# Kernel tuning notes

Measured on AMD Instinct MI355X. Metric: run time of the kernel, lower is better.

The kernel has to match this reference:

```python
import jax, jax.numpy as jnp
import numpy as np

N, DX, DZ, DY, H = 8192, 64, 128, 16, 512


def setup_inputs() -> dict:
    key = jax.random.key(0)
    ks = jax.random.split(key, 8)
    s1 = 1.0 / np.sqrt(DX)
    s2 = 1.0 / np.sqrt(H)
    return {
        "z_pred": jax.random.normal(ks[0], (N, DZ), dtype=jnp.float32),
        "x_label": jax.random.normal(ks[1], (N, DX), dtype=jnp.float32),
        "y_label": jax.random.normal(ks[2], (N, DY), dtype=jnp.float32),
        "W1": jax.random.normal(ks[3], (DX, H), dtype=jnp.float32) * s1,
        "b1": jnp.zeros((H,), dtype=jnp.float32),
        "W2": jax.random.normal(ks[4], (H, DZ), dtype=jnp.float32) * s2,
        "b2": jnp.zeros((DZ,), dtype=jnp.float32),
        "A": jax.random.normal(ks[5], (DZ, DZ), dtype=jnp.float32) * (1.0 / np.sqrt(DZ)),
        "B": jax.random.normal(ks[6], (DZ, DY), dtype=jnp.float32) * (1.0 / np.sqrt(DY)),
    }


def reference(z_pred, x_label, y_label, W1, b1, W2, b2, A, B):
    # forward_mapper T: x (dx,) -> (dz,), 2-layer tanh MLP
    def T(x):
        return jnp.tanh(x @ W1 + b1) @ W2 + b2

    # diff_eq: per-sample nonlinear dynamics x_dot = tanh(x)
    x_dot = jnp.tanh(x_label)  # (N, dx)

    # per-sample Jacobian dT/dx: (N, dz, dx). Equivalent to the torch code's
    # full N x N batched Jacobian followed by the diagonal slice, but without
    # the O(N^2) waste.
    jac = jax.vmap(jax.jacrev(T))(x_label)  # (N, dz, dx)

    dtdx_mul_f = jnp.einsum("nzd,nd->nz", jac, x_dot)  # (N, dz)
    m_mul_t = z_pred @ A.T                              # (N, dz)
    k_mul_h = y_label @ B.T                             # (N, dz)

    pde = dtdx_mul_f - m_mul_t - k_mul_h                # (N, dz)
    loss_batch = jnp.linalg.norm(pde, axis=1)           # (N,)
    return jnp.mean(loss_batch)
```

## Files before the change

### kernel.cpp

```cpp
#include <hip/hip_runtime.h>
#include <math.h>

#define Nn   8192
#define DXc  64
#define DZc  128
#define DYc  16
#define Hc   512
#define NKC  21

typedef short bf16x8 __attribute__((ext_vector_type(8)));
typedef float f32x4  __attribute__((ext_vector_type(4)));

__device__ __forceinline__ float fast_tanh(float x) {
    float e = __expf(2.0f * x);
    return 1.0f - 2.0f / (e + 1.0f);
}
__device__ __forceinline__ short f2bf(float f) {
    unsigned u = __float_as_uint(f);
    return (short)((u + 0x7FFFu + ((u >> 16) & 1u)) >> 16);
}
__device__ __forceinline__ bf16x8 pack8(float4 a, float4 b) {
    bf16x8 r;
    r[0]=f2bf(a.x); r[1]=f2bf(a.y); r[2]=f2bf(a.z); r[3]=f2bf(a.w);
    r[4]=f2bf(b.x); r[5]=f2bf(b.y); r[6]=f2bf(b.z); r[7]=f2bf(b.w);
    return r;
}

__global__ void prep_kernel(const float* __restrict__ W1,
                            const float* __restrict__ W2,
                            const float* __restrict__ A,
                            const float* __restrict__ Bm,
                            short* __restrict__ Wb,
                            short* __restrict__ Wf) {
    __shared__ float tile[64 * 129];
    const int blk = blockIdx.x, t = threadIdx.x;

    if (blk < 8) {
        const int jb = blk * 64;
#pragma unroll
        for (int p = 0; p < 16; p++) {
            int lin = p * 256 + t;
            int k = lin >> 6, jj = lin & 63;
            tile[jj * 65 + k] = W1[(size_t)k * Hc + jb + jj];
        }
        __syncthreads();
#pragma unroll
        for (int p = 0; p < 2; p++) {
            int cid = p * 256 + t;
            int lane = cid & 63, q = lane >> 4, n16 = lane & 15;
            int kc2 = (cid >> 6) & 1, jt4 = cid >> 7;
            int jl = jt4 * 16 + n16, k0 = kc2 * 32 + q * 8;
            bf16x8 v;
#pragma unroll
            for (int i = 0; i < 8; i++) v[i] = f2bf(tile[jl * 65 + k0 + i]);
            int block = ((blk * 4 + jt4) * 2 + kc2);
            *(bf16x8*)(Wb + (size_t)(block * 64 + lane) * 8) = v;
        }
    } else if (blk < 16) {
        const int kb = (blk - 8) * 64;
#pragma unroll
        for (int p = 0; p < 32; p++) {
            int lin = p * 256 + t;
            int kk = lin >> 7, z = lin & 127;
            tile[kk * 129 + z] = W2[(size_t)(kb + kk) * DZc + z];
        }
        __syncthreads();
#pragma unroll
        for (int p = 0; p < 4; p++) {
            int cid = p * 256 + t;
            int lane = cid & 63, q = lane >> 4, n16 = lane & 15;
            int rest = cid >> 6;
            int kc2 = rest & 1, zt = rest >> 1;
            int z = zt * 16 + n16, k0l = kc2 * 32 + q * 8;
            bf16x8 v;
#pragma unroll
            for (int i = 0; i < 8; i++) v[i] = f2bf(tile[(k0l + i) * 129 + z]);
            int kc = (kb >> 5) + kc2;
            *(bf16x8*)(Wf + (size_t)((zt * NKC + kc) * 64 + lane) * 8) = v;
        }
    } else if (blk < 24) {
        int cid = (blk - 16) * 256 + t;
        int lane = cid & 63, q = lane >> 4, n16 = lane & 15;
        int rest = cid >> 6;
        int kcl = rest & 3, zt = rest >> 2;
        int z = zt * 16 + n16, c0 = kcl * 32 + q * 8;
        float4 a0 = *(const float4*)(A + (size_t)z * DZc + c0);
        float4 a1 = *(const float4*)(A + (size_t)z * DZc + c0 + 4);
        bf16x8 v;
        v[0]=f2bf(-a0.x); v[1]=f2bf(-a0.y); v[2]=f2bf(-a0.z); v[3]=f2bf(-a0.w);
        v[4]=f2bf(-a1.x); v[5]=f2bf(-a1.y); v[6]=f2bf(-a1.z); v[7]=f2bf(-a1.w);
        *(bf16x8*)(Wf + (size_t)((zt * NKC + 16 + kcl) * 64 + lane) * 8) = v;
    } else {
#pragma unroll
        for (int p = 0; p < 2; p++) {
            int cid = p * 256 + t;
            int lane = cid & 63, q = lane >> 4, n16 = lane & 15;
            int zt = cid >> 6;
            int z = zt * 16 + n16;
            bf16x8 v = (bf16x8){0,0,0,0,0,0,0,0};
            if (q < 2) {
                float4 b0 = *(const float4*)(Bm + (size_t)z * DYc + q * 8);
                float4 b1 = *(const float4*)(Bm + (size_t)z * DYc + q * 8 + 4);
                v[0]=f2bf(-b0.x); v[1]=f2bf(-b0.y); v[2]=f2bf(-b0.z); v[3]=f2bf(-b0.w);
                v[4]=f2bf(-b1.x); v[5]=f2bf(-b1.y); v[6]=f2bf(-b1.z); v[7]=f2bf(-b1.w);
            }
            *(bf16x8*)(Wf + (size_t)((zt * NKC + 20) * 64 + lane) * 8) = v;
        }
    }
}

#define MFMA16(a, b, c) __builtin_amdgcn_mfma_f32_16x16x32_bf16((a), (b), (c), 0, 0, 0)

__global__ __launch_bounds__(512, 4)
void pde_main(const float* __restrict__ z_pred,
              const float* __restrict__ x_label,
              const float* __restrict__ y_label,
              const float* __restrict__ b1,
              const short* __restrict__ Wb,
              const short* __restrict__ Wf,
              float* __restrict__ out) {
    __shared__ __align__(16) short sS[16 * 512];
    __shared__ float red[8][16];

    const int tid  = threadIdx.x;
    const int w    = tid >> 6;
    const int lane = tid & 63;
    const int n16  = lane & 15;
    const int q    = lane >> 4;
    const int n0   = blockIdx.x * 16;

    const float* xp = x_label + (size_t)(n0 + n16) * DXc + q * 8;
    float4 x0 = *(const float4*)xp,        x1 = *(const float4*)(xp + 4);
    float4 x2 = *(const float4*)(xp + 32), x3 = *(const float4*)(xp + 36);
    bf16x8 ax0 = pack8(x0, x1), ax1 = pack8(x2, x3);
    bf16x8 at0, at1;
    {
        float v[16] = {x0.x,x0.y,x0.z,x0.w, x1.x,x1.y,x1.z,x1.w,
                       x2.x,x2.y,x2.z,x2.w, x3.x,x3.y,x3.z,x3.w};
#pragma unroll
        for (int i = 0; i < 8; i++) { at0[i] = f2bf(fast_tanh(v[i])); at1[i] = f2bf(fast_tanh(v[8 + i])); }
    }

#pragma unroll
    for (int t = 0; t < 4; t++) {
        const int jt = 4 * w + t;
        const short* bp = Wb + (size_t)(jt * 2 * 64 + lane) * 8;
        bf16x8 bw0 = *(const bf16x8*)bp;
        bf16x8 bw1 = *(const bf16x8*)(bp + 512);
        f32x4 h = (f32x4){0.f,0.f,0.f,0.f};
        f32x4 u = (f32x4){0.f,0.f,0.f,0.f};
        h = MFMA16(ax0, bw0, h);  h = MFMA16(ax1, bw1, h);
        u = MFMA16(at0, bw0, u);  u = MFMA16(at1, bw1, u);
        const float bj = b1[jt * 16 + n16];
        const int j = jt * 16 + n16;
        const int sbase = (j >> 5) * 512 + ((j >> 3) & 3) * 128 + (j & 7);
#pragma unroll
        for (int reg = 0; reg < 4; reg++) {
            float tv = fast_tanh(h[reg] + bj);
            float s  = (1.f - tv * tv) * u[reg];
            sS[sbase + (q * 4 + reg) * 8] = f2bf(s);
        }
    }

    const short* wfb = Wf + (size_t)(w * NKC * 64 + lane) * 8;
    f32x4 acc = (f32x4){0.f,0.f,0.f,0.f};
    {
        const float* zp = z_pred + (size_t)(n0 + n16) * DZc + q * 8;
#pragma unroll
        for (int kcl = 0; kcl < 4; kcl++) {
            float4 a0 = *(const float4*)(zp + kcl * 32);
            float4 a1 = *(const float4*)(zp + kcl * 32 + 4);
            bf16x8 az = pack8(a0, a1);
            bf16x8 bz = *(const bf16x8*)(wfb + (16 + kcl) * 512);
            acc = MFMA16(az, bz, acc);
        }
        bf16x8 ay = (bf16x8){0,0,0,0,0,0,0,0};
        if (q < 2) {
            const float* yp = y_label + (size_t)(n0 + n16) * DYc + q * 8;
            ay = pack8(*(const float4*)yp, *(const float4*)(yp + 4));
        }
        acc = MFMA16(ay, *(const bf16x8*)(wfb + 20 * 512), acc);
    }

    __syncthreads();

#pragma unroll
    for (int kc = 0; kc < 16; kc++) {
        bf16x8 sa = *(const bf16x8*)(sS + kc * 512 + lane * 8);
        bf16x8 bk = *(const bf16x8*)(wfb + kc * 512);
        acc = MFMA16(sa, bk, acc);
    }

#pragma unroll
    for (int reg = 0; reg < 4; reg++) {
        float sq = acc[reg] * acc[reg];
        sq += __shfl_xor(sq, 1);
        sq += __shfl_xor(sq, 2);
        sq += __shfl_xor(sq, 4);
        sq += __shfl_xor(sq, 8);
        if (n16 == 0) red[w][q * 4 + reg] = sq;
    }
    __syncthreads();

    if (tid < 16) {
        float tot = 0.f;
#pragma unroll
        for (int i = 0; i < 8; i++) tot += red[i][tid];
        float nrm = sqrtf(tot);
        nrm += __shfl_xor(nrm, 1);
        nrm += __shfl_xor(nrm, 2);
        nrm += __shfl_xor(nrm, 4);
        nrm += __shfl_xor(nrm, 8);
        if (tid == 0) atomicAdd(out, nrm * (1.0f / (float)Nn));
    }
}

extern "C" void kernel_launch(void* const* d_in, const int* in_sizes, int n_in,
                              void* d_out, int out_size, void* d_ws, size_t ws_size,
                              hipStream_t stream) {
    const float* z_pred  = (const float*)d_in[0];
    const float* x_label = (const float*)d_in[1];
    const float* y_label = (const float*)d_in[2];
    const float* W1      = (const float*)d_in[3];
    const float* b1      = (const float*)d_in[4];
    const float* W2      = (const float*)d_in[5];
    const float* A       = (const float*)d_in[7];
    const float* Bm      = (const float*)d_in[8];

    short* Wb = (short*)d_ws;
    short* Wf = Wb + 512 * DXc;

    hipMemsetAsync(d_out, 0, sizeof(float), stream);
    prep_kernel<<<25, 256, 0, stream>>>(W1, W2, A, Bm, Wb, Wf);
    pde_main<<<Nn / 16, 512, 0, stream>>>(z_pred, x_label, y_label, b1, Wb, Wf, (float*)d_out);
}
```

Before: 95.44 us.

## Halve block size to 4 waves, fold memset into prep kernel, prefetch weights

The main kernel now runs 256 threads per 16-row block. Each wave handles 8 hidden tiles in the first GEMM and two output z-tiles with two accumulators in the second, which raises per-wave work and MFMA ILP. The output zeroing moves from a separate hipMemsetAsync into the prep kernel, removing one launch. The first four Wf fragments are prefetched before the barrier to hide load latency. Register pressure rises with the doubled accumulators and prefetch buffers.

New measurement: 93.77 us. Within noise of the previous version (-1.7%).

```diff
diff --git a/kernel.cpp b/kernel.cpp
--- a/kernel.cpp
+++ b/kernel.cpp
@@ -31,7 +31,8 @@
                             const float* __restrict__ A,
                             const float* __restrict__ Bm,
                             short* __restrict__ Wb,
-                            short* __restrict__ Wf) {
+                            short* __restrict__ Wf,
+                            float* __restrict__ out) {
     __shared__ float tile[64 * 129];
     const int blk = blockIdx.x, t = threadIdx.x;
 
@@ -91,6 +92,7 @@
         v[4]=f2bf(-a1.x); v[5]=f2bf(-a1.y); v[6]=f2bf(-a1.z); v[7]=f2bf(-a1.w);
         *(bf16x8*)(Wf + (size_t)((zt * NKC + 16 + kcl) * 64 + lane) * 8) = v;
     } else {
+        if (t == 0) out[0] = 0.f;
 #pragma unroll
         for (int p = 0; p < 2; p++) {
             int cid = p * 256 + t;
@@ -111,7 +113,7 @@
 
 #define MFMA16(a, b, c) __builtin_amdgcn_mfma_f32_16x16x32_bf16((a), (b), (c), 0, 0, 0)
 
-__global__ __launch_bounds__(512, 4)
+__global__ __launch_bounds__(256, 4)
 void pde_main(const float* __restrict__ z_pred,
               const float* __restrict__ x_label,
               const float* __restrict__ y_label,
@@ -120,7 +122,7 @@
               const short* __restrict__ Wf,
               float* __restrict__ out) {
     __shared__ __align__(16) short sS[16 * 512];
-    __shared__ float red[8][16];
+    __shared__ float red[4][16];
 
     const int tid  = threadIdx.x;
     const int w    = tid >> 6;
@@ -142,8 +144,8 @@
     }
 
 #pragma unroll
-    for (int t = 0; t < 4; t++) {
-        const int jt = 4 * w + t;
+    for (int t = 0; t < 8; t++) {
+        const int jt = 8 * w + t;
         const short* bp = Wb + (size_t)(jt * 2 * 64 + lane) * 8;
         bf16x8 bw0 = *(const bf16x8*)bp;
         bf16x8 bw1 = *(const bf16x8*)(bp + 512);
@@ -162,8 +164,10 @@
         }
     }
 
-    const short* wfb = Wf + (size_t)(w * NKC * 64 + lane) * 8;
-    f32x4 acc = (f32x4){0.f,0.f,0.f,0.f};
+    const short* wf0 = Wf + (size_t)((2 * w)     * NKC * 64 + lane) * 8;
+    const short* wf1 = Wf + (size_t)((2 * w + 1) * NKC * 64 + lane) * 8;
+    f32x4 acc0 = (f32x4){0.f,0.f,0.f,0.f};
+    f32x4 acc1 = (f32x4){0.f,0.f,0.f,0.f};
     {
         const float* zp = z_pred + (size_t)(n0 + n16) * DZc + q * 8;
 #pragma unroll
@@ -171,15 +175,23 @@
             float4 a0 = *(const float4*)(zp + kcl * 32);
             float4 a1 = *(const float4*)(zp + kcl * 32 + 4);
             bf16x8 az = pack8(a0, a1);
-            bf16x8 bz = *(const bf16x8*)(wfb + (16 + kcl) * 512);
-            acc = MFMA16(az, bz, acc);
+            acc0 = MFMA16(az, *(const bf16x8*)(wf0 + (16 + kcl) * 512), acc0);
+            acc1 = MFMA16(az, *(const bf16x8*)(wf1 + (16 + kcl) * 512), acc1);
         }
         bf16x8 ay = (bf16x8){0,0,0,0,0,0,0,0};
         if (q < 2) {
             const float* yp = y_label + (size_t)(n0 + n16) * DYc + q * 8;
             ay = pack8(*(const float4*)yp, *(const float4*)(yp + 4));
         }
-        acc = MFMA16(ay, *(const bf16x8*)(wfb + 20 * 512), acc);
+        acc0 = MFMA16(ay, *(const bf16x8*)(wf0 + 20 * 512), acc0);
+        acc1 = MFMA16(ay, *(const bf16x8*)(wf1 + 20 * 512), acc1);
+    }
+
+    bf16x8 pf0[4], pf1[4];
+#pragma unroll
+    for (int c = 0; c < 4; c++) {
+        pf0[c] = *(const bf16x8*)(wf0 + c * 512);
+        pf1[c] = *(const bf16x8*)(wf1 + c * 512);
     }
 
     __syncthreads();
@@ -187,13 +199,15 @@
 #pragma unroll
     for (int kc = 0; kc < 16; kc++) {
         bf16x8 sa = *(const bf16x8*)(sS + kc * 512 + lane * 8);
-        bf16x8 bk = *(const bf16x8*)(wfb + kc * 512);
-        acc = MFMA16(sa, bk, acc);
+        bf16x8 b0 = (kc < 4) ? pf0[kc & 3] : *(const bf16x8*)(wf0 + kc * 512);
+        bf16x8 b1f = (kc < 4) ? pf1[kc & 3] : *(const bf16x8*)(wf1 + kc * 512);
+        acc0 = MFMA16(sa, b0, acc0);
+        acc1 = MFMA16(sa, b1f, acc1);
     }
 
 #pragma unroll
     for (int reg = 0; reg < 4; reg++) {
-        float sq = acc[reg] * acc[reg];
+        float sq = fmaf(acc0[reg], acc0[reg], acc1[reg] * acc1[reg]);
         sq += __shfl_xor(sq, 1);
         sq += __shfl_xor(sq, 2);
         sq += __shfl_xor(sq, 4);
@@ -203,9 +217,7 @@
     __syncthreads();
 
     if (tid < 16) {
-        float tot = 0.f;
-#pragma unroll
-        for (int i = 0; i < 8; i++) tot += red[i][tid];
+        float tot = red[0][tid] + red[1][tid] + red[2][tid] + red[3][tid];
         float nrm = sqrtf(tot);
         nrm += __shfl_xor(nrm, 1);
         nrm += __shfl_xor(nrm, 2);
@@ -230,7 +242,6 @@
     short* Wb = (short*)d_ws;
     short* Wf = Wb + 512 * DXc;
 
-    hipMemsetAsync(d_out, 0, sizeof(float), stream);
-    prep_kernel<<<25, 256, 0, stream>>>(W1, W2, A, Bm, Wb, Wf);
-    pde_main<<<Nn / 16, 512, 0, stream>>>(z_pred, x_label, y_label, b1, Wb, Wf, (float*)d_out);
-}
+    prep_kernel<<<25, 256, 0, stream>>>(W1, W2, A, Bm, Wb, Wf, (float*)d_out);
+    pde_main<<<Nn / 16, 256, 0, stream>>>(z_pred, x_label, y_label, b1, Wb, Wf, (float*)d_out);
+}
```
